# Optimization experiments

Hardware: AMD Instinct MI355X
Metric: run time of the kernel (lower is better)

## Reference

```python
import jax, jax.numpy as jnp
import numpy as np


def _kernel_features(data, proj, is_query):
    # data: [B,S,H,D], proj: [R,D] -> features [B,S,H,R]  (FAVOR+ positive softmax kernel)
    d = data.shape[-1]
    r = proj.shape[0]
    data_normalizer = 1.0 / jnp.sqrt(jnp.sqrt(jnp.float32(d)))
    ratio = 1.0 / jnp.sqrt(jnp.float32(r))
    data_hat = jnp.einsum('bshd,rd->bshr', data_normalizer * data, proj)
    diag = (jnp.sum(data * data, axis=-1) * 0.5) * (data_normalizer * data_normalizer)
    diag = diag[..., None]  # [B,S,H,1]
    if is_query:
        m = jnp.max(data_hat, axis=-1, keepdims=True)
    else:
        m = jnp.max(data_hat)
    return ratio * (jnp.exp(data_hat - diag - m) + 1e-4)


def reference(query, key, value, Wq, bq, Wk, bk, Wv, bv, Wo, bo, proj):
    proj = jax.lax.stop_gradient(proj)
    # QKV projections: [B,S,Dm] -> [B,S,H,Dh]
    q = jnp.einsum('bsd,dhk->bshk', query, Wq) + bq
    k = jnp.einsum('bsd,dhk->bshk', key, Wk) + bk
    v = jnp.einsum('bsd,dhv->bshv', value, Wv) + bv
    q_hat = _kernel_features(q, proj, True)   # [B,S,H,R]
    k_hat = _kernel_features(k, proj, False)  # [B,S,H,R]
    # kv aggregation: 'aecr,aecd->acrd'
    kv = jnp.einsum('bshr,bshv->bhrv', k_hat, v)          # [B,H,R,Dv]
    out = jnp.einsum('bshr,bhrv->bshv', q_hat, kv)        # [B,S,H,Dv]
    # normalization: k1 = sum_s k_hat ('abcd,abc->acd'), denom = q_hat . k1
    k1 = jnp.sum(k_hat, axis=1)                           # [B,H,R]
    denom = jnp.einsum('bshr,bhr->bsh', q_hat, k1)        # [B,S,H]
    out = out / denom[..., None]
    # output projection: combine heads
    return jnp.einsum('bshv,hvd->bsd', out, Wo) + bo


def setup_inputs() -> dict:
    key0 = jax.random.key(0)
    ks = jax.random.split(key0, 10)
    B, S, Dm, H, Dh, R = 4, 4096, 1024, 16, 64, 256
    scale = 1.0 / np.sqrt(Dm)
    # Gaussian orthogonal random matrix [R, Dh], scaling=0 (chi row norms)
    blk = jax.random.normal(ks[8], (R, Dh))
    qmat, _ = jnp.linalg.qr(blk)  # R >= Dh -> q is [R, Dh]
    mult = jnp.linalg.norm(jax.random.normal(ks[9], (R, Dh)), axis=1)
    proj = mult[:, None] * qmat
    return {
        'query': jax.random.normal(ks[0], (B, S, Dm)),
        'key': jax.random.normal(ks[1], (B, S, Dm)),
        'value': jax.random.normal(ks[2], (B, S, Dm)),
        'Wq': jax.random.normal(ks[3], (Dm, H, Dh)) * scale,
        'bq': jnp.zeros((H, Dh)),
        'Wk': jax.random.normal(ks[4], (Dm, H, Dh)) * scale,
        'bk': jnp.zeros((H, Dh)),
        'Wv': jax.random.normal(ks[5], (Dm, H, Dh)) * scale,
        'bv': jnp.zeros((H, Dh)),
        'Wo': jax.random.normal(ks[6], (H, Dh, Dm)) * scale,
        'bo': jnp.zeros((Dm,)),
        'proj': proj,
    }
```

## Files before the change

kernel.cpp:

```cpp
#include <hip/hip_runtime.h>

typedef unsigned short u16;
typedef unsigned int u32;
typedef __attribute__((ext_vector_type(4))) float f32x4;
typedef __attribute__((ext_vector_type(8))) short bf16x8;

#define B_ 4
#define S_ 4096
#define H_ 16
#define DH_ 64
#define R_ 256
#define DM_ 1024
#define M_ 16384
#define ROWSTR 1024

__device__ __forceinline__ float bf2f(u16 u) {
  union { u32 i; float f; } v; v.i = ((u32)u) << 16; return v.f;
}
__device__ __forceinline__ u16 f2bf(float f) {
  union { float f; u32 i; } v; v.f = f;
  u32 x = v.i;
  return (u16)((x + 0x7FFFu + ((x >> 16) & 1u)) >> 16);
}
__device__ __forceinline__ void lds_load16(const void* g, void* l) {
  __builtin_amdgcn_global_load_lds((__attribute__((address_space(1))) void*)(g),
                                   (__attribute__((address_space(3))) void*)(l), 16, 0, 0);
}
__device__ __forceinline__ int vt_idx(int dv, int s) {
  return dv * 64 + (s ^ (dv & 0x38));
}

__global__ __launch_bounds__(256) void dtype_probe_k(const u16* __restrict__ q,
                                                     int* __restrict__ flag) {
  __shared__ int cnt_s;
  int tid = threadIdx.x;
  if (tid == 0) cnt_s = 0;
  __syncthreads();
  int c = 0;
  for (int i = tid; i < 1024; i += 256) {
    u32 e = ((u32)q[i] >> 7) & 0xFF;
    c += (e >= 134) ? 1 : 0;
  }
  atomicAdd(&cnt_s, c);
  __syncthreads();
  if (tid == 0) flag[0] = (cnt_s > 32) ? 1 : 0;
}

template <int WLO>
__global__ __launch_bounds__(256) void split_k(const void* __restrict__ src,
                                               u16* __restrict__ hi, u16* __restrict__ lo,
                                               const int* __restrict__ flag) {
  const bool f32m = flag[0] != 0;
  size_t i = ((size_t)blockIdx.x * 256 + threadIdx.x) * 8;
  if (f32m) {
    f32x4 a = *(const f32x4*)((const float*)src + i);
    f32x4 b = *(const f32x4*)((const float*)src + i + 4);
    bf16x8 h, l;
    for (int e = 0; e < 4; ++e) {
      u16 ha = f2bf(a[e]); h[e] = (short)ha; l[e] = (short)f2bf(a[e] - bf2f(ha));
      u16 hb = f2bf(b[e]); h[4 + e] = (short)hb; l[4 + e] = (short)f2bf(b[e] - bf2f(hb));
    }
    *(bf16x8*)(hi + i) = h;
    if (WLO) *(bf16x8*)(lo + i) = l;
  } else {
    bf16x8 h = *(const bf16x8*)((const u16*)src + i);
    *(bf16x8*)(hi + i) = h;
    if (WLO) {
      bf16x8 z = {0, 0, 0, 0, 0, 0, 0, 0};
      *(bf16x8*)(lo + i) = z;
    }
  }
}

__global__ __launch_bounds__(256) void transpose4_k(
    const void* __restrict__ s0, const void* __restrict__ s1,
    const void* __restrict__ s2, const void* __restrict__ s3,
    u16* __restrict__ dh0, u16* __restrict__ dl0, u16* __restrict__ dh1, u16* __restrict__ dl1,
    u16* __restrict__ dh2, u16* __restrict__ dl2, u16* __restrict__ dh3, u16* __restrict__ dl3,
    const int* __restrict__ flag) {
  __shared__ float tile[32][33];
  const bool f32m = flag[0] != 0;
  int z = blockIdx.z;
  const void* src = (z == 0) ? s0 : (z == 1) ? s1 : (z == 2) ? s2 : s3;
  u16* dh = (z == 0) ? dh0 : (z == 1) ? dh1 : (z == 2) ? dh2 : dh3;
  u16* dl = (z == 0) ? dl0 : (z == 1) ? dl1 : (z == 2) ? dl2 : dl3;
  int tx = threadIdx.x, ty = threadIdx.y;
  int x0 = blockIdx.x * 32, y0 = blockIdx.y * 32;
  for (int i = ty; i < 32; i += 8) {
    size_t idx = (size_t)(y0 + i) * DM_ + x0 + tx;
    tile[i][tx] = f32m ? ((const float*)src)[idx] : bf2f(((const u16*)src)[idx]);
  }
  __syncthreads();
  for (int i = ty; i < 32; i += 8) {
    float t = tile[tx][i];
    u16 hi = f2bf(t);
    size_t o = (size_t)(x0 + i) * DM_ + y0 + tx;
    dh[o] = hi;
    dl[o] = f2bf(t - bf2f(hi));
  }
}

__global__ __launch_bounds__(256) void projcvt_k(const void* __restrict__ p,
                                                 u16* __restrict__ ph, u16* __restrict__ pl,
                                                 const int* __restrict__ flag) {
  const bool f32m = flag[0] != 0;
  int i = blockIdx.x * 256 + threadIdx.x;
  if (i < R_ * DH_) {
    float t = f32m ? ((const float*)p)[i] : bf2f(((const u16*)p)[i]);
    u16 hi = f2bf(t);
    ph[i] = hi;
    pl[i] = f2bf(t - bf2f(hi));
  }
}

template <int PREC, int OUTMODE>
__global__ __launch_bounds__(256) void gemm_k(
    const u16* __restrict__ Ah, const u16* __restrict__ Al,
    const u16* __restrict__ Bth, const u16* __restrict__ Btl,
    const void* __restrict__ bias, void* __restrict__ C, u16* __restrict__ Clo,
    float* __restrict__ diag, const int* __restrict__ flag) {
  constexpr int NPL = (PREC == 3) ? 4 : 2;
  __shared__ __attribute__((aligned(16))) u16 pool[2 * NPL * 4096];
  const bool f32m = flag[0] != 0;
  const int K = DM_, N = DM_;
  const int tid = threadIdx.x, wave = tid >> 6, lane = tid & 63;
  const int lr = lane & 15, qd = lane >> 4;
  const int bm = blockIdx.x, bn = blockIdx.y;
  const int m0 = (wave & 1) * 64, n0 = (wave >> 1) * 64;
  const u16* Abh = Ah + (size_t)bm * 128 * K;
  const u16* Bbh = Bth + (size_t)bn * 128 * K;
  const u16* Abl = (PREC == 3) ? Al + (size_t)bm * 128 * K : nullptr;
  const u16* Bbl = (PREC == 3) ? Btl + (size_t)bn * 128 * K : nullptr;
  f32x4 zero = {0.f, 0.f, 0.f, 0.f};
  f32x4 acc[4][4];
  for (int i = 0; i < 4; ++i) for (int j = 0; j < 4; ++j) acc[i][j] = zero;

#define GEMM_STAGE(bf, kk)                                             \
  do {                                                                 \
    u16* Ph_ = pool + (bf) * (NPL * 4096);                             \
    for (int t_ = 0; t_ < 2; ++t_) {                                   \
      int c_ = wave + t_ * 4;                                          \
      int row_ = c_ * 16 + (lane >> 2);                                \
      int kc_ = (lane & 3) * 8;                                        \
      size_t go_ = (size_t)row_ * K + (kk) + kc_;                      \
      lds_load16(Abh + go_, (void*)&Ph_[c_ * 512]);                    \
      lds_load16(Bbh + go_, (void*)&Ph_[4096 + c_ * 512]);             \
      if (PREC == 3) {                                                 \
        lds_load16(Abl + go_, (void*)&Ph_[2 * 4096 + c_ * 512]);       \
        lds_load16(Bbl + go_, (void*)&Ph_[3 * 4096 + c_ * 512]);       \
      }                                                                \
    }                                                                  \
  } while (0)

  GEMM_STAGE(0, 0);
  int cur = 0;
  for (int k0 = 0; k0 < K; k0 += 32) {
    __syncthreads();
    if (k0 + 32 < K) GEMM_STAGE(cur ^ 1, k0 + 32);
    const u16* Ph = pool + cur * (NPL * 4096);
    const u16* Ash = Ph;
    const u16* Bsh = Ph + 4096;
    bf16x8 ah[4], bh[4];
    for (int i = 0; i < 4; ++i) ah[i] = *(const bf16x8*)&Ash[(m0 + i * 16 + lr) * 32 + qd * 8];
    for (int j = 0; j < 4; ++j) bh[j] = *(const bf16x8*)&Bsh[(n0 + j * 16 + lr) * 32 + qd * 8];
    for (int i = 0; i < 4; ++i)
      for (int j = 0; j < 4; ++j)
        acc[i][j] = __builtin_amdgcn_mfma_f32_16x16x32_bf16(ah[i], bh[j], acc[i][j], 0, 0, 0);
    if (PREC == 3) {
      const u16* Asl = Ph + 2 * 4096;
      const u16* Bsl = Ph + 3 * 4096;
      bf16x8 al[4], bl[4];
      for (int i = 0; i < 4; ++i) al[i] = *(const bf16x8*)&Asl[(m0 + i * 16 + lr) * 32 + qd * 8];
      for (int j = 0; j < 4; ++j) bl[j] = *(const bf16x8*)&Bsl[(n0 + j * 16 + lr) * 32 + qd * 8];
      for (int i = 0; i < 4; ++i)
        for (int j = 0; j < 4; ++j) {
          acc[i][j] = __builtin_amdgcn_mfma_f32_16x16x32_bf16(ah[i], bl[j], acc[i][j], 0, 0, 0);
          acc[i][j] = __builtin_amdgcn_mfma_f32_16x16x32_bf16(al[i], bh[j], acc[i][j], 0, 0, 0);
        }
    }
    cur ^= 1;
  }
#undef GEMM_STAGE
  float dq[16];
  if (OUTMODE == 1)
    for (int t = 0; t < 16; ++t) dq[t] = 0.f;
  for (int j = 0; j < 4; ++j) {
    int n = bn * 128 + n0 + j * 16 + lr;
    float bv = f32m ? ((const float*)bias)[n] : bf2f(((const u16*)bias)[n]);
    for (int i = 0; i < 4; ++i) {
      int mr = bm * 128 + m0 + i * 16 + qd * 4;
      for (int r2 = 0; r2 < 4; ++r2) {
        float x = acc[i][j][r2] + bv;
        size_t o = (size_t)(mr + r2) * N + n;
        if (OUTMODE == 0) {
          ((u16*)C)[o] = f2bf(x);
        } else if (OUTMODE == 1) {
          dq[i * 4 + r2] += x * x;
          u16 hi = f2bf(x);
          ((u16*)C)[o] = hi;
          Clo[o] = f2bf(x - bf2f(hi));
        } else {
          if (f32m) ((float*)C)[o] = x;
          else ((u16*)C)[o] = f2bf(x);
        }
      }
    }
  }
  if (OUTMODE == 1) {
    int h = (bn * 128 + n0) >> 6;
    for (int t = 0; t < 16; ++t) {
      float v = dq[t];
      v += __shfl_xor(v, 1, 64); v += __shfl_xor(v, 2, 64);
      v += __shfl_xor(v, 4, 64); v += __shfl_xor(v, 8, 64);
      if (lr == 0) {
        int mrow = bm * 128 + m0 + (t >> 2) * 16 + qd * 4 + (t & 3);
        diag[(size_t)mrow * H_ + h] = 0.0625f * v;
      }
    }
  }
}

__global__ __launch_bounds__(256) void reduce_max_k(const float* __restrict__ pm,
                                                    float* __restrict__ mout, int n) {
  __shared__ float buf[256];
  int t = threadIdx.x;
  float m = -3.0e38f;
  for (int i = t; i < n; i += 256) m = fmaxf(m, pm[i]);
  buf[t] = m;
  __syncthreads();
  if (t < 64) {
    float v = fmaxf(fmaxf(buf[t], buf[t + 64]), fmaxf(buf[t + 128], buf[t + 192]));
    for (int m2 = 1; m2 < 64; m2 <<= 1) v = fmaxf(v, __shfl_xor(v, m2, 64));
    if (t == 0) mout[0] = v;
  }
}

__global__ __launch_bounds__(256) void kv_accum_k(
    const u16* __restrict__ khi, const u16* __restrict__ klo,
    const u16* __restrict__ vv,
    const u16* __restrict__ ph, const u16* __restrict__ pl,
    const float* __restrict__ diagk,
    float* __restrict__ pkv, float* __restrict__ pk1,
    float* __restrict__ pvs, float* __restrict__ pmc, int ipb) {
  __shared__ __attribute__((aligned(16))) u16 pool[256 * 72];
  __shared__ __attribute__((aligned(16))) u16 vTh[64 * 64];
  __shared__ float diagl[64];
  __shared__ float red[4];
  u16* kth = pool;
  u16* ktl = pool + 4096;
  u16* khatT = pool;
  const int tid = threadIdx.x, wave = tid >> 6, lane = tid & 63;
  const int lr = lane & 15, qd = lane >> 4;
  int bid = blockIdx.x;
  int bh = bid & 63, c = bid >> 6;
  int b = bh >> 4, h = bh & 15;
  const float nrm = 0.3535533905932738f;
  size_t base0 = (((size_t)b * S_ + (size_t)c * ipb * 64) * H_ + h) * DH_;
  int grow0 = b * S_ + c * ipb * 64;
  f32x4 zero = {0.f, 0.f, 0.f, 0.f};
  f32x4 acc[4][4];
  for (int i = 0; i < 4; ++i) for (int j = 0; j < 4; ++j) acc[i][j] = zero;
  float k1p[4][4];
  for (int i = 0; i < 4; ++i) for (int r2 = 0; r2 < 4; ++r2) k1p[i][r2] = 0.f;
  float mr = -3.0e38f;
  float vs[16];
  for (int e = 0; e < 16; ++e) vs[e] = 0.f;
  const int r0 = wave * 64;
  bf16x8 pfa_h[2][4], pfa_l[2][4];
  for (int ks = 0; ks < 2; ++ks)
    for (int i = 0; i < 4; ++i) {
      size_t o = (size_t)(r0 + i * 16 + lr) * DH_ + ks * 32 + qd * 8;
      pfa_h[ks][i] = *(const bf16x8*)(ph + o);
      pfa_l[ks][i] = *(const bf16x8*)(pl + o);
    }
  for (int it = 0; it < ipb; ++it) {
    size_t ibase = base0 + (size_t)it * 64 * ROWSTR;
    __syncthreads();
    for (int t = 0; t < 2; ++t) {
      int cc = wave + t * 4;
      int rr = cc * 8 + (lane >> 3);
      int csw = (((lane & 7) ^ (rr & 7)) << 3);
      size_t go = ibase + (size_t)rr * ROWSTR + csw;
      lds_load16(khi + go, (void*)&kth[cc * 512]);
      lds_load16(klo + go, (void*)&ktl[cc * 512]);
    }
    if (tid < 64) diagl[tid] = diagk[(size_t)(grow0 + it * 64 + tid) * H_ + h];
    {
      int s = tid >> 2;
      int dv0 = (tid & 3) * 16;
      size_t go = ibase + (size_t)s * ROWSTR + dv0;
      bf16x8 h0 = *(const bf16x8*)(vv + go);
      bf16x8 h1 = *(const bf16x8*)(vv + go + 8);
      for (int e = 0; e < 8; ++e) {
        vTh[vt_idx(dv0 + e, s)] = (u16)h0[e];
        vTh[vt_idx(dv0 + 8 + e, s)] = (u16)h1[e];
        vs[e] += bf2f((u16)h0[e]);
        vs[8 + e] += bf2f((u16)h1[e]);
      }
    }
    __syncthreads();
    f32x4 a1[4][4];
    for (int i = 0; i < 4; ++i) for (int j = 0; j < 4; ++j) a1[i][j] = zero;
    __builtin_amdgcn_s_setprio(1);
    for (int ks = 0; ks < 2; ++ks) {
      bf16x8 bh_[4], bl_[4];
      for (int j = 0; j < 4; ++j) {
        int cof = (ks * 32 + qd * 8) ^ ((lr & 7) << 3);
        bh_[j] = *(const bf16x8*)&kth[(j * 16 + lr) * 64 + cof];
        bl_[j] = *(const bf16x8*)&ktl[(j * 16 + lr) * 64 + cof];
      }
      for (int i = 0; i < 4; ++i)
        for (int j = 0; j < 4; ++j) {
          a1[i][j] = __builtin_amdgcn_mfma_f32_16x16x32_bf16(pfa_h[ks][i], bh_[j], a1[i][j], 0, 0, 0);
          a1[i][j] = __builtin_amdgcn_mfma_f32_16x16x32_bf16(pfa_l[ks][i], bh_[j], a1[i][j], 0, 0, 0);
          a1[i][j] = __builtin_amdgcn_mfma_f32_16x16x32_bf16(pfa_h[ks][i], bl_[j], a1[i][j], 0, 0, 0);
        }
    }
    __builtin_amdgcn_s_setprio(0);
    float mx = -3.0e38f;
    for (int i = 0; i < 4; ++i) for (int j = 0; j < 4; ++j) for (int r2 = 0; r2 < 4; ++r2)
      mx = fmaxf(mx, a1[i][j][r2]);
    for (int m2 = 1; m2 < 64; m2 <<= 1) mx = fmaxf(mx, __shfl_xor(mx, m2, 64));
    if (lane == 0) red[wave] = mx;
    __syncthreads();
    float cm = nrm * fmaxf(fmaxf(red[0], red[1]), fmaxf(red[2], red[3]));
    if (cm > mr) {
      float sc = __expf(mr - cm);
      for (int i = 0; i < 4; ++i) for (int j = 0; j < 4; ++j)
        for (int r2 = 0; r2 < 4; ++r2) acc[i][j][r2] *= sc;
      for (int i = 0; i < 4; ++i) for (int r2 = 0; r2 < 4; ++r2) k1p[i][r2] *= sc;
      mr = cm;
    }
    for (int i = 0; i < 4; ++i)
      for (int r2 = 0; r2 < 4; ++r2) {
        int r = r0 + i * 16 + qd * 4 + r2;
        for (int j = 0; j < 4; ++j) {
          int s = j * 16 + lr;
          float arg = nrm * a1[i][j][r2] - diagl[s] - mr;
          u16 khb = f2bf(__expf(arg));
          khatT[r * 72 + s] = khb;
          k1p[i][r2] += bf2f(khb);
        }
      }
    __syncthreads();
    __builtin_amdgcn_s_setprio(1);
    for (int ks = 0; ks < 2; ++ks) {
      bf16x8 af[4], bh_[4];
      for (int i = 0; i < 4; ++i)
        af[i] = *(const bf16x8*)&khatT[(r0 + i * 16 + lr) * 72 + ks * 32 + qd * 8];
      for (int j = 0; j < 4; ++j) {
        int dv = j * 16 + lr;
        bh_[j] = *(const bf16x8*)&vTh[vt_idx(dv, ks * 32 + qd * 8)];
      }
      for (int i = 0; i < 4; ++i)
        for (int j = 0; j < 4; ++j)
          acc[i][j] = __builtin_amdgcn_mfma_f32_16x16x32_bf16(af[i], bh_[j], acc[i][j], 0, 0, 0);
    }
    __builtin_amdgcn_s_setprio(0);
  }
  size_t obase = ((size_t)c * 64 + bh) * R_;
  for (int i = 0; i < 4; ++i)
    for (int j = 0; j < 4; ++j)
      for (int r2 = 0; r2 < 4; ++r2) {
        int r = r0 + i * 16 + qd * 4 + r2;
        int dv = j * 16 + lr;
        pkv[(obase + r) * DH_ + dv] = acc[i][j][r2];
      }
  for (int i = 0; i < 4; ++i)
    for (int r2 = 0; r2 < 4; ++r2) {
      float v = k1p[i][r2];
      v += __shfl_xor(v, 1, 64); v += __shfl_xor(v, 2, 64);
      v += __shfl_xor(v, 4, 64); v += __shfl_xor(v, 8, 64);
      if (lr == 0) pk1[obase + r0 + i * 16 + qd * 4 + r2] = v;
    }
  if (tid == 0) pmc[bid] = mr;
  __syncthreads();
  float* fbuf = (float*)pool;
  {
    int srow = tid >> 2, g = tid & 3;
    for (int e = 0; e < 16; ++e) fbuf[srow * 64 + g * 16 + e] = vs[e];
  }
  __syncthreads();
  if (tid < 64) {
    float s = 0.f;
    for (int r = 0; r < 64; ++r) s += fbuf[r * 64 + tid];
    pvs[(size_t)bid * 64 + tid] = s;
  }
}

__global__ __launch_bounds__(256) void kv_reduce_k(
    const float* __restrict__ pkv, const float* __restrict__ pk1,
    const float* __restrict__ pvs, const float* __restrict__ pmc,
    const float* __restrict__ mg,
    u16* __restrict__ kvTh, u16* __restrict__ kvTl, float* __restrict__ k1, int nchunk) {
  __shared__ float tile[64][65];
  __shared__ float wbuf[16];
  __shared__ float vbuf[64];
  int bh = blockIdx.x, tl = blockIdx.y, t = threadIdx.x;
  const float ratio = 0.0625f;
  float mg0 = mg[0];
  if (t < nchunk) wbuf[t] = __expf(pmc[(size_t)t * 64 + bh] - mg0);
  if (t >= 64 && t < 128) {
    int dv = t - 64;
    float s = 0.f;
    for (int c2 = 0; c2 < nchunk; ++c2) s += pvs[((size_t)c2 * 64 + bh) * 64 + dv];
    vbuf[dv] = s;
  }
  __syncthreads();
  if (tl == 0) {
    float s = 0.f;
    for (int c2 = 0; c2 < nchunk; ++c2)
      s += wbuf[c2] * pk1[((size_t)c2 * 64 + bh) * R_ + t];
    k1[(size_t)bh * R_ + t] = ratio * (s + 1e-4f * (float)S_);
  }
  for (int e = 0; e < 16; ++e) {
    int idx = e * 256 + t;
    int rl = idx >> 6, dv = idx & 63;
    float s = 0.f;
    for (int c2 = 0; c2 < nchunk; ++c2)
      s += wbuf[c2] * pkv[(((size_t)c2 * 64 + bh) * R_ + tl * 64 + rl) * DH_ + dv];
    tile[rl][dv] = ratio * (s + 1e-4f * vbuf[dv]);
  }
  __syncthreads();
  for (int e = 0; e < 16; ++e) {
    int idx = e * 256 + t;
    int dv = idx >> 6, rl = idx & 63;
    float s = tile[rl][dv];
    u16 hi = f2bf(s);
    size_t o = ((size_t)bh * DH_ + dv) * R_ + tl * 64 + rl;
    kvTh[o] = hi;
    kvTl[o] = f2bf(s - bf2f(hi));
  }
}

__global__ __launch_bounds__(256, 4) void q_out_k(
    const u16* __restrict__ qhi, const u16* __restrict__ qlo,
    const u16* __restrict__ ph, const u16* __restrict__ pl,
    const u16* __restrict__ kvTh, const u16* __restrict__ kvTl,
    const float* __restrict__ k1, const float* __restrict__ diagq,
    u16* __restrict__ op) {
  __shared__ __attribute__((aligned(16))) u16 pool[64 * 264];
  __shared__ float wrm[4][64];
  __shared__ float dpart[4][64];
  __shared__ float diagl[64];
  __shared__ float dinv[64];
  u16* qth = pool;
  u16* qtl = pool + 4096;
  u16* qh = pool;
  const int tid = threadIdx.x, wave = tid >> 6, lane = tid & 63;
  const int lr = lane & 15, qd = lane >> 4;
  int bid = blockIdx.x;
  int chunk = bid & 63, bh = bid >> 6;
  int b = bh >> 4, h = bh & 15;
  const float nrm = 0.3535533905932738f;
  const float ratio = 0.0625f;
  size_t base = (((size_t)b * S_ + (size_t)chunk * 64) * H_ + h) * DH_;
  const u16* kvThb = kvTh + (size_t)bh * DH_ * R_;
  const u16* kvTlb = kvTl + (size_t)bh * DH_ * R_;
  const float* k1b = k1 + (size_t)bh * R_;
  for (int t = 0; t < 2; ++t) {
    int cc = wave + t * 4;
    int rr = cc * 8 + (lane >> 3);
    int csw = (((lane & 7) ^ (rr & 7)) << 3);
    size_t go = base + (size_t)rr * ROWSTR + csw;
    lds_load16(qhi + go, (void*)&qth[cc * 512]);
    lds_load16(qlo + go, (void*)&qtl[cc * 512]);
  }
  if (tid < 64) diagl[tid] = diagq[(size_t)(b * S_ + chunk * 64 + tid) * H_ + h];
  __syncthreads();
  f32x4 zero = {0.f, 0.f, 0.f, 0.f};
  f32x4 a1[4][4];
  for (int i = 0; i < 4; ++i) for (int j = 0; j < 4; ++j) a1[i][j] = zero;
  const int r0 = wave * 64;
  __builtin_amdgcn_s_setprio(1);
  for (int ks = 0; ks < 2; ++ks) {
    bf16x8 ah[4], al[4], bh_[4], bl_[4];
    for (int i = 0; i < 4; ++i) {
      int cof = (ks * 32 + qd * 8) ^ ((lr & 7) << 3);
      ah[i] = *(const bf16x8*)&qth[(i * 16 + lr) * 64 + cof];
      al[i] = *(const bf16x8*)&qtl[(i * 16 + lr) * 64 + cof];
    }
    for (int j = 0; j < 4; ++j) {
      size_t o = (size_t)(r0 + j * 16 + lr) * DH_ + ks * 32 + qd * 8;
      bh_[j] = *(const bf16x8*)(ph + o);
      bl_[j] = *(const bf16x8*)(pl + o);
    }
    for (int i = 0; i < 4; ++i)
      for (int j = 0; j < 4; ++j) {
        a1[i][j] = __builtin_amdgcn_mfma_f32_16x16x32_bf16(ah[i], bh_[j], a1[i][j], 0, 0, 0);
        a1[i][j] = __builtin_amdgcn_mfma_f32_16x16x32_bf16(al[i], bh_[j], a1[i][j], 0, 0, 0);
        a1[i][j] = __builtin_amdgcn_mfma_f32_16x16x32_bf16(ah[i], bl_[j], a1[i][j], 0, 0, 0);
      }
  }
  __builtin_amdgcn_s_setprio(0);
  for (int i = 0; i < 4; ++i)
    for (int r2 = 0; r2 < 4; ++r2) {
      float v = fmaxf(fmaxf(a1[i][0][r2], a1[i][1][r2]), fmaxf(a1[i][2][r2], a1[i][3][r2]));
      v = fmaxf(v, __shfl_xor(v, 1, 64)); v = fmaxf(v, __shfl_xor(v, 2, 64));
      v = fmaxf(v, __shfl_xor(v, 4, 64)); v = fmaxf(v, __shfl_xor(v, 8, 64));
      if (lr == 0) wrm[wave][i * 16 + qd * 4 + r2] = v;
    }
  __syncthreads();
  float k1v[4];
  for (int j = 0; j < 4; ++j) k1v[j] = k1b[r0 + j * 16 + lr];
  for (int i = 0; i < 4; ++i)
    for (int r2 = 0; r2 < 4; ++r2) {
      int s = i * 16 + qd * 4 + r2;
      float rmax = fmaxf(fmaxf(wrm[0][s], wrm[1][s]), fmaxf(wrm[2][s], wrm[3][s]));
      float dg = diagl[s];
      float dsum = 0.f;
      for (int j = 0; j < 4; ++j) {
        float arg = nrm * (a1[i][j][r2] - rmax) - dg;
        float qv = ratio * (__expf(arg) + 1e-4f);
        u16 qvb = f2bf(qv);
        qh[s * 264 + r0 + j * 16 + lr] = qvb;
        dsum += bf2f(qvb) * k1v[j];
      }
      dsum += __shfl_xor(dsum, 1, 64);
      dsum += __shfl_xor(dsum, 2, 64);
      dsum += __shfl_xor(dsum, 4, 64);
      dsum += __shfl_xor(dsum, 8, 64);
      if (lr == 0) dpart[wave][s] = dsum;
    }
  __syncthreads();
  if (tid < 64) {
    float dn = dpart[0][tid] + dpart[1][tid] + dpart[2][tid] + dpart[3][tid];
    dinv[tid] = 1.0f / fmaxf(dn, 1e-35f);
  }
  __syncthreads();
  f32x4 a2[2][2];
  for (int i = 0; i < 2; ++i) for (int j = 0; j < 2; ++j) a2[i][j] = zero;
  const int sw2 = (wave & 1) * 32, dw = (wave >> 1) * 32;
  __builtin_amdgcn_s_setprio(1);
  for (int ks = 0; ks < 8; ++ks) {
    bf16x8 af[2], bh_[2], bl_[2];
    for (int i = 0; i < 2; ++i)
      af[i] = *(const bf16x8*)&qh[(sw2 + i * 16 + lr) * 264 + ks * 32 + qd * 8];
    for (int j = 0; j < 2; ++j) {
      size_t o = (size_t)(dw + j * 16 + lr) * R_ + ks * 32 + qd * 8;
      bh_[j] = *(const bf16x8*)(kvThb + o);
      bl_[j] = *(const bf16x8*)(kvTlb + o);
    }
    for (int i = 0; i < 2; ++i)
      for (int j = 0; j < 2; ++j) {
        a2[i][j] = __builtin_amdgcn_mfma_f32_16x16x32_bf16(af[i], bh_[j], a2[i][j], 0, 0, 0);
        a2[i][j] = __builtin_amdgcn_mfma_f32_16x16x32_bf16(af[i], bl_[j], a2[i][j], 0, 0, 0);
      }
  }
  __builtin_amdgcn_s_setprio(0);
  for (int i = 0; i < 2; ++i)
    for (int r2 = 0; r2 < 4; ++r2) {
      int s = sw2 + i * 16 + qd * 4 + r2;
      float di = dinv[s];
      for (int j = 0; j < 2; ++j) {
        int dv = dw + j * 16 + lr;
        op[base + (size_t)s * ROWSTR + dv] = f2bf(a2[i][j][r2] * di);
      }
    }
}

extern "C" void kernel_launch(void* const* d_in, const int* in_sizes, int n_in,
                              void* d_out, int out_size, void* d_ws, size_t ws_size,
                              hipStream_t stream) {
  const void* query = d_in[0];
  const void* key   = d_in[1];
  const void* value = d_in[2];
  const void* Wq = d_in[3];
  const void* bq = d_in[4];
  const void* Wk = d_in[5];
  const void* bk = d_in[6];
  const void* Wv = d_in[7];
  const void* bv = d_in[8];
  const void* Wo = d_in[9];
  const void* bo = d_in[10];
  const void* proj = d_in[11];

  char* w = (char*)d_ws;
  const size_t MB = 1024 * 1024;
  u16* WqT_h = (u16*)(w + 0 * MB);
  u16* WqT_l = (u16*)(w + 2 * MB);
  u16* WkT_h = (u16*)(w + 4 * MB);
  u16* WkT_l = (u16*)(w + 6 * MB);
  u16* WvT_h = (u16*)(w + 8 * MB);
  u16* WvT_l = (u16*)(w + 10 * MB);
  u16* WoT_h = (u16*)(w + 12 * MB);
  u16* WoT_l = (u16*)(w + 14 * MB);
  u16* kq_hi = (u16*)(w + 16 * MB);
  u16* kq_lo = (u16*)(w + 48 * MB);
  u16* vop   = (u16*)(w + 80 * MB);
  float* pvs = (float*)(w + 112 * MB);
  u16* kvTh  = (u16*)(w + 112 * MB + 512 * 1024);
  u16* kvTl  = (u16*)(w + 114 * MB + 512 * 1024);
  float* k1  = (float*)(w + 116 * MB + 512 * 1024);
  float* pmc = (float*)(w + 116 * MB + 640 * 1024);
  float* mg  = (float*)(w + 116 * MB + 700 * 1024);
  u16* p_hi  = (u16*)(w + 116 * MB + 768 * 1024);
  u16* p_lo  = (u16*)(w + 116 * MB + 832 * 1024);
  int* flag  = (int*)(w + 116 * MB + 900 * 1024);
  float* pkv  = (float*)(w + 117 * MB);
  u16* inA_hi = (u16*)(w + 117 * MB);
  u16* inA_lo = (u16*)(w + 149 * MB);
  float* diag_b = (float*)(w + 181 * MB);
  float* pk1b   = (float*)(w + 182 * MB);
  int nchunk = 16;
  int ipb = 64 / nchunk;

  dtype_probe_k<<<1, 256, 0, stream>>>((const u16*)query, flag);
  transpose4_k<<<dim3(32, 32, 4), dim3(32, 8), 0, stream>>>(
      Wq, Wk, Wv, Wo, WqT_h, WqT_l, WkT_h, WkT_l, WvT_h, WvT_l, WoT_h, WoT_l, flag);
  projcvt_k<<<64, 256, 0, stream>>>(proj, p_hi, p_lo, flag);
  split_k<1><<<8192, 256, 0, stream>>>(key, inA_hi, inA_lo, flag);
  gemm_k<3, 1><<<dim3(128, 8), 256, 0, stream>>>(inA_hi, inA_lo, WkT_h, WkT_l, bk, kq_hi, kq_lo, diag_b, flag);
  split_k<0><<<8192, 256, 0, stream>>>(value, inA_hi, nullptr, flag);
  gemm_k<1, 0><<<dim3(128, 8), 256, 0, stream>>>(inA_hi, nullptr, WvT_h, nullptr, bv, vop, nullptr, nullptr, flag);
  kv_accum_k<<<nchunk * 64, 256, 0, stream>>>(kq_hi, kq_lo, vop, p_hi, p_lo, diag_b, pkv, pk1b, pvs, pmc, ipb);
  reduce_max_k<<<1, 256, 0, stream>>>(pmc, mg, nchunk * 64);
  kv_reduce_k<<<dim3(64, 4), 256, 0, stream>>>(pkv, pk1b, pvs, pmc, mg, kvTh, kvTl, k1, nchunk);
  split_k<1><<<8192, 256, 0, stream>>>(query, inA_hi, inA_lo, flag);
  gemm_k<3, 1><<<dim3(128, 8), 256, 0, stream>>>(inA_hi, inA_lo, WqT_h, WqT_l, bq, kq_hi, kq_lo, diag_b, flag);
  q_out_k<<<4096, 256, 0, stream>>>(kq_hi, kq_lo, p_hi, p_lo, kvTh, kvTl, k1, diag_b, vop);
  gemm_k<1, 2><<<dim3(128, 8), 256, 0, stream>>>(vop, nullptr, WoT_h, nullptr, bo, d_out, nullptr, nullptr, flag);
}
```

Before: 863.0 us.

## Serialize split-precision GEMM passes, fuse global max into kv_reduce, halve chunks

The 3-pass bf16 split GEMM now streams hi*hi, hi*lo and lo*hi as three sequential K sweeps through a two-plane LDS double buffer, instead of loading four planes per k-step. This halves LDS use per block and should allow higher occupancy, at the cost of reloading the A/B hi tiles. The separate single-block max-reduction kernel is folded into kv_reduce_k, which drops one launch but makes every block redo the small max scan. The kv accumulation chunk count drops from 16 to 8, and the transpose skips writing low halves for Wv and Wo, which are never read.

```diff
diff --git a/kernel.cpp b/kernel.cpp
--- a/kernel.cpp
+++ b/kernel.cpp
@@ -96,7 +96,7 @@
     u16 hi = f2bf(t);
     size_t o = (size_t)(x0 + i) * DM_ + y0 + tx;
     dh[o] = hi;
-    dl[o] = f2bf(t - bf2f(hi));
+    if (z < 2) dl[o] = f2bf(t - bf2f(hi));
   }
 }
 
@@ -119,10 +119,10 @@
     const u16* __restrict__ Bth, const u16* __restrict__ Btl,
     const void* __restrict__ bias, void* __restrict__ C, u16* __restrict__ Clo,
     float* __restrict__ diag, const int* __restrict__ flag) {
-  constexpr int NPL = (PREC == 3) ? 4 : 2;
-  __shared__ __attribute__((aligned(16))) u16 pool[2 * NPL * 4096];
+  __shared__ __attribute__((aligned(16))) u16 pool[2 * 2 * 4096];
   const bool f32m = flag[0] != 0;
   const int K = DM_, N = DM_;
+  constexpr int KT = (PREC == 3) ? 96 : 32;
   const int tid = threadIdx.x, wave = tid >> 6, lane = tid & 63;
   const int lr = lane & 15, qd = lane >> 4;
   const int bm = blockIdx.x, bn = blockIdx.y;
@@ -135,49 +135,36 @@
   f32x4 acc[4][4];
   for (int i = 0; i < 4; ++i) for (int j = 0; j < 4; ++j) acc[i][j] = zero;
 
-#define GEMM_STAGE(bf, kk)                                             \
+#define GEMM_STAGE(bf, t)                                              \
   do {                                                                 \
-    u16* Ph_ = pool + (bf) * (NPL * 4096);                             \
+    int seg_ = (PREC == 3) ? ((t) >> 5) : 0;                           \
+    int kk_ = ((t) & 31) * 32;                                         \
+    const u16* Ap_ = (seg_ == 2) ? Abl : Abh;                          \
+    const u16* Bp_ = (seg_ == 1) ? Bbl : Bbh;                          \
+    u16* Ph_ = pool + (bf) * 8192;                                     \
     for (int t_ = 0; t_ < 2; ++t_) {                                   \
       int c_ = wave + t_ * 4;                                          \
       int row_ = c_ * 16 + (lane >> 2);                                \
       int kc_ = (lane & 3) * 8;                                        \
-      size_t go_ = (size_t)row_ * K + (kk) + kc_;                      \
-      lds_load16(Abh + go_, (void*)&Ph_[c_ * 512]);                    \
-      lds_load16(Bbh + go_, (void*)&Ph_[4096 + c_ * 512]);             \
-      if (PREC == 3) {                                                 \
-        lds_load16(Abl + go_, (void*)&Ph_[2 * 4096 + c_ * 512]);       \
-        lds_load16(Bbl + go_, (void*)&Ph_[3 * 4096 + c_ * 512]);       \
-      }                                                                \
+      size_t go_ = (size_t)row_ * K + kk_ + kc_;                       \
+      lds_load16(Ap_ + go_, (void*)&Ph_[c_ * 512]);                    \
+      lds_load16(Bp_ + go_, (void*)&Ph_[4096 + c_ * 512]);             \
     }                                                                  \
   } while (0)
 
   GEMM_STAGE(0, 0);
   int cur = 0;
-  for (int k0 = 0; k0 < K; k0 += 32) {
+  for (int t = 0; t < KT; ++t) {
     __syncthreads();
-    if (k0 + 32 < K) GEMM_STAGE(cur ^ 1, k0 + 32);
-    const u16* Ph = pool + cur * (NPL * 4096);
-    const u16* Ash = Ph;
-    const u16* Bsh = Ph + 4096;
+    if (t + 1 < KT) GEMM_STAGE(cur ^ 1, t + 1);
+    const u16* Ash = pool + cur * 8192;
+    const u16* Bsh = Ash + 4096;
     bf16x8 ah[4], bh[4];
     for (int i = 0; i < 4; ++i) ah[i] = *(const bf16x8*)&Ash[(m0 + i * 16 + lr) * 32 + qd * 8];
     for (int j = 0; j < 4; ++j) bh[j] = *(const bf16x8*)&Bsh[(n0 + j * 16 + lr) * 32 + qd * 8];
     for (int i = 0; i < 4; ++i)
       for (int j = 0; j < 4; ++j)
         acc[i][j] = __builtin_amdgcn_mfma_f32_16x16x32_bf16(ah[i], bh[j], acc[i][j], 0, 0, 0);
-    if (PREC == 3) {
-      const u16* Asl = Ph + 2 * 4096;
-      const u16* Bsl = Ph + 3 * 4096;
-      bf16x8 al[4], bl[4];
-      for (int i = 0; i < 4; ++i) al[i] = *(const bf16x8*)&Asl[(m0 + i * 16 + lr) * 32 + qd * 8];
-      for (int j = 0; j < 4; ++j) bl[j] = *(const bf16x8*)&Bsl[(n0 + j * 16 + lr) * 32 + qd * 8];
-      for (int i = 0; i < 4; ++i)
-        for (int j = 0; j < 4; ++j) {
-          acc[i][j] = __builtin_amdgcn_mfma_f32_16x16x32_bf16(ah[i], bl[j], acc[i][j], 0, 0, 0);
-          acc[i][j] = __builtin_amdgcn_mfma_f32_16x16x32_bf16(al[i], bh[j], acc[i][j], 0, 0, 0);
-        }
-    }
     cur ^= 1;
   }
 #undef GEMM_STAGE
@@ -217,21 +204,6 @@
         diag[(size_t)mrow * H_ + h] = 0.0625f * v;
       }
     }
-  }
-}
-
-__global__ __launch_bounds__(256) void reduce_max_k(const float* __restrict__ pm,
-                                                    float* __restrict__ mout, int n) {
-  __shared__ float buf[256];
-  int t = threadIdx.x;
-  float m = -3.0e38f;
-  for (int i = t; i < n; i += 256) m = fmaxf(m, pm[i]);
-  buf[t] = m;
-  __syncthreads();
-  if (t < 64) {
-    float v = fmaxf(fmaxf(buf[t], buf[t + 64]), fmaxf(buf[t + 128], buf[t + 192]));
-    for (int m2 = 1; m2 < 64; m2 <<= 1) v = fmaxf(v, __shfl_xor(v, m2, 64));
-    if (t == 0) mout[0] = v;
   }
 }
 
@@ -391,14 +363,23 @@
 __global__ __launch_bounds__(256) void kv_reduce_k(
     const float* __restrict__ pkv, const float* __restrict__ pk1,
     const float* __restrict__ pvs, const float* __restrict__ pmc,
-    const float* __restrict__ mg,
     u16* __restrict__ kvTh, u16* __restrict__ kvTl, float* __restrict__ k1, int nchunk) {
   __shared__ float tile[64][65];
   __shared__ float wbuf[16];
   __shared__ float vbuf[64];
+  __shared__ float mgs;
   int bh = blockIdx.x, tl = blockIdx.y, t = threadIdx.x;
   const float ratio = 0.0625f;
-  float mg0 = mg[0];
+  {
+    float m = -3.0e38f;
+    for (int i = t; i < nchunk * 64; i += 256) m = fmaxf(m, pmc[i]);
+    for (int m2 = 1; m2 < 64; m2 <<= 1) m = fmaxf(m, __shfl_xor(m, m2, 64));
+    if ((t & 63) == 0) tile[0][t >> 6] = m;
+    __syncthreads();
+    if (t == 0) mgs = fmaxf(fmaxf(tile[0][0], tile[0][1]), fmaxf(tile[0][2], tile[0][3]));
+    __syncthreads();
+  }
+  float mg0 = mgs;
   if (t < nchunk) wbuf[t] = __expf(pmc[(size_t)t * 64 + bh] - mg0);
   if (t >= 64 && t < 128) {
     int dv = t - 64;
@@ -593,7 +574,6 @@
   u16* kvTl  = (u16*)(w + 114 * MB + 512 * 1024);
   float* k1  = (float*)(w + 116 * MB + 512 * 1024);
   float* pmc = (float*)(w + 116 * MB + 640 * 1024);
-  float* mg  = (float*)(w + 116 * MB + 700 * 1024);
   u16* p_hi  = (u16*)(w + 116 * MB + 768 * 1024);
   u16* p_lo  = (u16*)(w + 116 * MB + 832 * 1024);
   int* flag  = (int*)(w + 116 * MB + 900 * 1024);
@@ -602,7 +582,7 @@
   u16* inA_lo = (u16*)(w + 149 * MB);
   float* diag_b = (float*)(w + 181 * MB);
   float* pk1b   = (float*)(w + 182 * MB);
-  int nchunk = 16;
+  int nchunk = 8;
   int ipb = 64 / nchunk;
 
   dtype_probe_k<<<1, 256, 0, stream>>>((const u16*)query, flag);
@@ -614,8 +594,7 @@
   split_k<0><<<8192, 256, 0, stream>>>(value, inA_hi, nullptr, flag);
   gemm_k<1, 0><<<dim3(128, 8), 256, 0, stream>>>(inA_hi, nullptr, WvT_h, nullptr, bv, vop, nullptr, nullptr, flag);
   kv_accum_k<<<nchunk * 64, 256, 0, stream>>>(kq_hi, kq_lo, vop, p_hi, p_lo, diag_b, pkv, pk1b, pvs, pmc, ipb);
-  reduce_max_k<<<1, 256, 0, stream>>>(pmc, mg, nchunk * 64);
-  kv_reduce_k<<<dim3(64, 4), 256, 0, stream>>>(pkv, pk1b, pvs, pmc, mg, kvTh, kvTl, k1, nchunk);
+  kv_reduce_k<<<dim3(64, 4), 256, 0, stream>>>(pkv, pk1b, pvs, pmc, kvTh, kvTl, k1, nchunk);
   split_k<1><<<8192, 256, 0, stream>>>(query, inA_hi, inA_lo, flag);
   gemm_k<3, 1><<<dim3(128, 8), 256, 0, stream>>>(inA_hi, inA_lo, WqT_h, WqT_l, bq, kq_hi, kq_lo, diag_b, flag);
   q_out_k<<<4096, 256, 0, stream>>>(kq_hi, kq_lo, p_hi, p_lo, kvTh, kvTl, k1, diag_b, vop);
```

Result: no change. 869.7 us (+0.8%).
